# Performance work log

Measured on AMD Instinct MI355X. Metric: run time of the kernel, lower is better.

Reference implementation:

```python
import jax, jax.numpy as jnp
import numpy as np

HEAD_DIM = 1024
SCALE = HEAD_DIM ** -0.25  # qk_scale defaults to exponent -0.25


def setup_inputs() -> dict:
    key = jax.random.key(0)
    ks = jax.random.split(key, 6)
    B_s, B_q, C = 4096, 4096, 1024
    return {
        "query": jax.random.normal(ks[0], (B_q, C), dtype=jnp.float32),
        "s": jax.random.normal(ks[1], (B_s, C), dtype=jnp.float32),
        "TG_prompt": jax.random.normal(ks[2], (B_s, C), dtype=jnp.float32),
        "W_qkv": jax.random.normal(ks[3], (3 * HEAD_DIM, C), dtype=jnp.float32) * (C ** -0.5),
        "W_proj_s": jax.random.normal(ks[4], (HEAD_DIM, HEAD_DIM), dtype=jnp.float32) * (HEAD_DIM ** -0.5),
        "W_proj_q": jax.random.normal(ks[5], (HEAD_DIM, HEAD_DIM), dtype=jnp.float32) * (HEAD_DIM ** -0.5),
    }


def reference(query, s, TG_prompt, W_qkv, W_proj_s, W_proj_q):
    B_s = s.shape[0]
    t = s + TG_prompt                       # [B_s, C]
    c = jnp.concatenate([t, query], axis=0)  # [B, C], B = B_s + B_q
    x = c @ W_qkv.T                          # [B, 3*head_dim]
    q, k, v = jnp.split(x, 3, axis=-1)       # each [B, head_dim]
    # separate sqrt-scale on q and k, then full [B, B] scores
    attn = jax.nn.softmax((q * SCALE) @ (k.T * SCALE), axis=-1)
    attn_cq = attn[:B_s, B_s:]               # [B_s, B_q]
    attn_qc = attn[B_s:, :B_s]               # [B_q, B_s]
    # matmul against raw query / s (NOT v), then per-branch projection
    x_s = (attn_cq @ query) @ W_proj_s.T     # [B_s, head_dim]
    x_q = (attn_qc @ s) @ W_proj_q.T         # [B_q, head_dim]
    return (x_s, x_q)
```

## Files before the change

kernel.cpp:

```cpp
#include <hip/hip_runtime.h>


typedef unsigned short u16;
typedef __bf16 bf16x8 __attribute__((ext_vector_type(8)));
typedef float f32x4 __attribute__((ext_vector_type(4)));
typedef unsigned short u16x8 __attribute__((ext_vector_type(8)));

#define DEVI static __device__ __forceinline__

DEVI u16 f2b(float f) {
  unsigned int u = __float_as_uint(f);
  u += 0x7fffu + ((u >> 16) & 1u);
  return (u16)(u >> 16);
}

DEVI float exp2_hw(float x) {
  float r;
  asm("v_exp_f32 %0, %1" : "=v"(r) : "v"(x));
  return r;
}

__global__ void prep_all(const float* __restrict__ query, const float* __restrict__ s,
                         const float* __restrict__ tg, const float* __restrict__ w0,
                         const float* __restrict__ w1, const float* __restrict__ w2,
                         u16* __restrict__ cB, u16* __restrict__ sBf,
                         u16* __restrict__ o0, u16* __restrict__ o1,
                         u16* __restrict__ o2, float* __restrict__ rowsum) {
  int b = blockIdx.x;
  if (b >= 6144) {
    rowsum[(b - 6144) * 1024 + (int)threadIdx.x * 4 + 0] = 0.f;
    rowsum[(b - 6144) * 1024 + (int)threadIdx.x * 4 + 1] = 0.f;
    rowsum[(b - 6144) * 1024 + (int)threadIdx.x * 4 + 2] = 0.f;
    rowsum[(b - 6144) * 1024 + (int)threadIdx.x * 4 + 3] = 0.f;
    return;
  }
  if (b < 4096) {
    int base = (b * 256 + threadIdx.x) << 3;
    int row = base >> 10;
    u16x8 o;
    if (row < 4096) {
      float4 a0 = *(const float4*)(s + base);
      float4 a1 = *(const float4*)(s + base + 4);
      float4 b0 = *(const float4*)(tg + base);
      float4 b1 = *(const float4*)(tg + base + 4);
      u16x8 os;
      os[0] = f2b(a0.x); os[1] = f2b(a0.y); os[2] = f2b(a0.z); os[3] = f2b(a0.w);
      os[4] = f2b(a1.x); os[5] = f2b(a1.y); os[6] = f2b(a1.z); os[7] = f2b(a1.w);
      *(u16x8*)(sBf + base) = os;
      o[0] = f2b(a0.x + b0.x); o[1] = f2b(a0.y + b0.y);
      o[2] = f2b(a0.z + b0.z); o[3] = f2b(a0.w + b0.w);
      o[4] = f2b(a1.x + b1.x); o[5] = f2b(a1.y + b1.y);
      o[6] = f2b(a1.z + b1.z); o[7] = f2b(a1.w + b1.w);
    } else {
      int qb = base - 4096 * 1024;
      float4 a0 = *(const float4*)(query + qb);
      float4 a1 = *(const float4*)(query + qb + 4);
      o[0] = f2b(a0.x); o[1] = f2b(a0.y); o[2] = f2b(a0.z); o[3] = f2b(a0.w);
      o[4] = f2b(a1.x); o[5] = f2b(a1.y); o[6] = f2b(a1.z); o[7] = f2b(a1.w);
    }
    *(u16x8*)(cB + base) = o;
  } else {
    const float* in; u16* out; int lb;
    if (b < 5120)      { in = w0; out = o0; lb = b - 4096; }
    else if (b < 5632) { in = w1; out = o1; lb = b - 5120; }
    else               { in = w2; out = o2; lb = b - 5632; }
    int base = (lb * 256 + threadIdx.x) << 3;
    float4 a0 = *(const float4*)(in + base);
    float4 a1 = *(const float4*)(in + base + 4);
    u16x8 o;
    o[0] = f2b(a0.x); o[1] = f2b(a0.y); o[2] = f2b(a0.z); o[3] = f2b(a0.w);
    o[4] = f2b(a1.x); o[5] = f2b(a1.y); o[6] = f2b(a1.z); o[7] = f2b(a1.w);
    *(u16x8*)(out + base) = o;
  }
}

__global__ __launch_bounds__(256)
void gemm_qkv(const u16* __restrict__ cB, const u16* __restrict__ WqkB,
              u16* __restrict__ qks,
              const u16* __restrict__ WpsB, const u16* __restrict__ WpqB,
              const u16* __restrict__ qBf, const u16* __restrict__ sBf,
              u16* __restrict__ VsT, u16* __restrict__ VqT,
              float sq, float sk) {
  __shared__ __align__(16) u16 sA[128 * 64];
  __shared__ __align__(16) u16 sB[128 * 64];
  const int b = blockIdx.x;
  const u16* Ap; const u16* Bp; u16* op;
  int bx, by, ldc;
  bool proj;
  if (b < 1024) {
    proj = true;  bx = b & 15; by = b >> 4;
    Ap = cB; Bp = WqkB; op = qks; ldc = 2048;
  } else {
    proj = false;
    int b2 = b - 1024;
    int z = b2 >> 8, rem = b2 & 255;
    bx = rem & 31; by = rem >> 5;
    Ap = z ? WpqB : WpsB; Bp = z ? sBf : qBf; op = z ? VqT : VsT; ldc = 4096;
  }
  const int tid = threadIdx.x;
  const int lane = tid & 63;
  const int wave = tid >> 6;
  const int wr = (wave >> 1) * 64;
  const int wc = (wave & 1) * 64;
  const int ar = lane & 15;

  const u16* Ab = Ap + (size_t)(by * 128) * 1024;
  const u16* Bb = Bp + (size_t)(bx * 128) * 1024;

  f32x4 zero = {0.0f, 0.0f, 0.0f, 0.0f};
  f32x4 acc[4][4];
#pragma unroll
  for (int i = 0; i < 4; ++i)
#pragma unroll
    for (int j = 0; j < 4; ++j) acc[i][j] = zero;

  const int sr = tid >> 3;
  const int scL = (tid & 7) << 3;
  const int scG = ((tid & 7) ^ (sr & 7)) << 3;

  const int l7 = lane & 7, l16 = lane >> 4;
  const int p0b = (l16 ^ l7) << 4;
  const int offA0 = (wr + ar) * 128 + p0b;
  const int offB0 = (wc + ar) * 128 + p0b;
  const char* sAc = (const char*)sA;
  const char* sBc = (const char*)sB;

  for (int k0 = 0; k0 < 1024; k0 += 64) {
#pragma unroll
    for (int it = 0; it < 4; ++it) {
      int r = it * 32 + sr;
      __builtin_amdgcn_global_load_lds(
          (__attribute__((address_space(1))) void*)(Ab + (size_t)r * 1024 + k0 + scG),
          (__attribute__((address_space(3))) void*)(sA + r * 64 + scL), 16, 0, 0);
    }
#pragma unroll
    for (int it = 0; it < 4; ++it) {
      int r = it * 32 + sr;
      __builtin_amdgcn_global_load_lds(
          (__attribute__((address_space(1))) void*)(Bb + (size_t)r * 1024 + k0 + scG),
          (__attribute__((address_space(3))) void*)(sB + r * 64 + scL), 16, 0, 0);
    }
    __syncthreads();
#pragma unroll
    for (int half = 0; half < 2; ++half) {
      const int px = half ? 64 : 0;
      bf16x8 af[4], bfr[4];
#pragma unroll
      for (int t = 0; t < 4; ++t)
        af[t] = *(const bf16x8*)(sAc + ((offA0 ^ px) + t * 2048));
#pragma unroll
      for (int t = 0; t < 4; ++t)
        bfr[t] = *(const bf16x8*)(sBc + ((offB0 ^ px) + t * 2048));
#pragma unroll
      for (int tm = 0; tm < 4; ++tm)
#pragma unroll
        for (int tn = 0; tn < 4; ++tn)
          acc[tm][tn] = __builtin_amdgcn_mfma_f32_16x16x32_bf16(
              af[tm], bfr[tn], acc[tm][tn], 0, 0, 0);
    }
    __syncthreads();
  }

  const int qr = (lane >> 4) * 4;
  const int qc = lane & 15;
#pragma unroll
  for (int tm = 0; tm < 4; ++tm)
#pragma unroll
    for (int r = 0; r < 4; ++r) {
      int row = by * 128 + wr + tm * 16 + qr + r;
#pragma unroll
      for (int tn = 0; tn < 4; ++tn) {
        int col = bx * 128 + wc + tn * 16 + qc;
        float sc = proj ? ((col < 1024) ? sq : sk) : 1.0f;
        op[(size_t)row * ldc + col] = f2b(acc[tm][tn][r] * sc);
      }
    }
}


template <int EPI>
__global__ __launch_bounds__(256)
void gemm_bt(const u16* __restrict__ A, const u16* __restrict__ A1,
             const u16* __restrict__ B, const u16* __restrict__ B1,
             int lda, int ldb, int K, int ldc,
             float* __restrict__ outf, float* __restrict__ outf1,
             const float* __restrict__ rs, const float* __restrict__ rs1,
             u16* __restrict__ Pcq, u16* __restrict__ Pqc,
             float* __restrict__ rowsum) {
  __shared__ __align__(16) u16 sA[128 * 64];
  __shared__ __align__(16) u16 sB[128 * 64];
  const int tid = threadIdx.x;
  const int lane = tid & 63;
  const int wave = tid >> 6;
  const int wr = (wave >> 1) * 64;
  const int wc = (wave & 1) * 64;
  const int ar = lane & 15;
  const int by = blockIdx.y, bx = blockIdx.x;
  const int z = blockIdx.z;

  const u16* Ab = (z ? A1 : A) + (size_t)(by * 128) * lda;
  const u16* Bb = (z ? B1 : B) + (size_t)(bx * 128) * ldb;

  f32x4 zero = {0.0f, 0.0f, 0.0f, 0.0f};
  f32x4 acc[4][4];
#pragma unroll
  for (int i = 0; i < 4; ++i)
#pragma unroll
    for (int j = 0; j < 4; ++j) acc[i][j] = zero;

  const int sr = tid >> 3;
  const int scL = (tid & 7) << 3;
  const int scG = ((tid & 7) ^ (sr & 7)) << 3;

  const int l7 = lane & 7, l16 = lane >> 4;
  const int p0b = (l16 ^ l7) << 4;
  const int offA0 = (wr + ar) * 128 + p0b;
  const int offB0 = (wc + ar) * 128 + p0b;
  const char* sAc = (const char*)sA;
  const char* sBc = (const char*)sB;

  for (int k0 = 0; k0 < K; k0 += 64) {
#pragma unroll
    for (int it = 0; it < 4; ++it) {
      int r = it * 32 + sr;
      __builtin_amdgcn_global_load_lds(
          (__attribute__((address_space(1))) void*)(Ab + (size_t)r * lda + k0 + scG),
          (__attribute__((address_space(3))) void*)(sA + r * 64 + scL), 16, 0, 0);
    }
#pragma unroll
    for (int it = 0; it < 4; ++it) {
      int r = it * 32 + sr;
      __builtin_amdgcn_global_load_lds(
          (__attribute__((address_space(1))) void*)(Bb + (size_t)r * ldb + k0 + scG),
          (__attribute__((address_space(3))) void*)(sB + r * 64 + scL), 16, 0, 0);
    }
    __syncthreads();
#pragma unroll
    for (int half = 0; half < 2; ++half) {
      const int px = half ? 64 : 0;
      bf16x8 af[4], bfr[4];
#pragma unroll
      for (int t = 0; t < 4; ++t)
        af[t] = *(const bf16x8*)(sAc + ((offA0 ^ px) + t * 2048));
#pragma unroll
      for (int t = 0; t < 4; ++t)
        bfr[t] = *(const bf16x8*)(sBc + ((offB0 ^ px) + t * 2048));
#pragma unroll
      for (int tm = 0; tm < 4; ++tm)
#pragma unroll
        for (int tn = 0; tn < 4; ++tn)
          acc[tm][tn] = __builtin_amdgcn_mfma_f32_16x16x32_bf16(
              af[tm], bfr[tn], acc[tm][tn], 0, 0, 0);
    }
    __syncthreads();
  }

  const int qr = (lane >> 4) * 4;
  const int qc = lane & 15;

  if constexpr (EPI == 1) {
    const bool top = (by < 32);
    const bool left = (bx < 32);
    u16* pdst = nullptr;
    if (top && !left) pdst = Pcq;
    if (!top && left) pdst = Pqc;
    const int growb = by * 128 + wr;
    const int rbase = growb - (top ? 0 : 4096);
    const int cbase = bx * 128 + wc - (left ? 0 : 4096);
#pragma unroll
    for (int tm = 0; tm < 4; ++tm) {
      float e[4][4];
      float rsum[4] = {0.f, 0.f, 0.f, 0.f};
#pragma unroll
      for (int tn = 0; tn < 4; ++tn)
#pragma unroll
        for (int r = 0; r < 4; ++r) {
          e[tn][r] = exp2_hw(acc[tm][tn][r]);
          rsum[r] += e[tn][r];
        }
#pragma unroll
      for (int r = 0; r < 4; ++r) {
        float v = rsum[r];
        v += __shfl_xor(v, 1);
        v += __shfl_xor(v, 2);
        v += __shfl_xor(v, 4);
        v += __shfl_xor(v, 8);
        if ((lane & 15) == 0)
          atomicAdd(&rowsum[growb + tm * 16 + qr + r], v);
      }
      if (pdst) {
#pragma unroll
        for (int tn = 0; tn < 4; ++tn)
#pragma unroll
          for (int r = 0; r < 4; ++r) {
            int row = rbase + tm * 16 + qr + r;
            pdst[(size_t)row * 4096 + cbase + tn * 16 + qc] = f2b(e[tn][r]);
          }
      }
    }
  } else {
    float* of = z ? outf1 : outf;
    const float* rsz = z ? rs1 : rs;
#pragma unroll
    for (int tm = 0; tm < 4; ++tm)
#pragma unroll
      for (int r = 0; r < 4; ++r) {
        int row = by * 128 + wr + tm * 16 + qr + r;
        float inv = 1.0f / rsz[row];
#pragma unroll
        for (int tn = 0; tn < 4; ++tn) {
          int col = bx * 128 + wc + tn * 16 + qc;
          of[(size_t)row * ldc + col] = acc[tm][tn][r] * inv;
        }
      }
  }
}


extern "C" void kernel_launch(void* const* d_in, const int* in_sizes, int n_in,
                              void* d_out, int out_size, void* d_ws, size_t ws_size,
                              hipStream_t stream) {
  (void)in_sizes; (void)n_in; (void)out_size; (void)ws_size;
  const float* query = (const float*)d_in[0];
  const float* s     = (const float*)d_in[1];
  const float* tg    = (const float*)d_in[2];
  const float* Wqkv  = (const float*)d_in[3];
  const float* Wps   = (const float*)d_in[4];
  const float* Wpq   = (const float*)d_in[5];
  float* out = (float*)d_out;

  char* ws = (char*)d_ws;
  u16* cB     = (u16*)ws; ws += (size_t)8192 * 1024 * 2;
  u16* sBf    = (u16*)ws; ws += (size_t)4096 * 1024 * 2;
  u16* qks    = (u16*)ws; ws += (size_t)8192 * 2048 * 2;
  u16* WqkB   = (u16*)ws; ws += (size_t)2048 * 1024 * 2;
  u16* WpsB   = (u16*)ws; ws += (size_t)1024 * 1024 * 2;
  u16* WpqB   = (u16*)ws; ws += (size_t)1024 * 1024 * 2;
  u16* VsT    = (u16*)ws; ws += (size_t)1024 * 4096 * 2;
  u16* VqT    = (u16*)ws; ws += (size_t)1024 * 4096 * 2;
  u16* Pcq    = (u16*)ws; ws += (size_t)4096 * 4096 * 2;
  u16* Pqc    = (u16*)ws; ws += (size_t)4096 * 4096 * 2;
  float* rowsum = (float*)ws;

  const u16* qBf = cB + (size_t)4096 * 1024;

  const float SCALE = 0.17677669529663687f;
  const float LOG2E = 1.4426950408889634f;

  prep_all<<<6152, 256, 0, stream>>>(query, s, tg, Wqkv, Wps, Wpq,
                                     cB, sBf, WqkB, WpsB, WpqB, rowsum);
  gemm_qkv<<<1536, 256, 0, stream>>>(cB, WqkB, qks, WpsB, WpqB, qBf, sBf,
                                     VsT, VqT, SCALE * LOG2E, SCALE);
  gemm_bt<1><<<dim3(64, 64), 256, 0, stream>>>(
      qks, nullptr, qks + 1024, nullptr, 2048, 2048, 1024, 0,
      nullptr, nullptr, nullptr, nullptr, Pcq, Pqc, rowsum);
  gemm_bt<4><<<dim3(8, 32, 2), 256, 0, stream>>>(
      Pcq, Pqc, VsT, VqT, 4096, 4096, 4096, 1024,
      out, out + (size_t)4096 * 1024, rowsum, rowsum + 4096,
      nullptr, nullptr, nullptr);
}
```

Baseline: 468.1 us.

## Enlarge GEMM block tiles to 256x128 with 8-wave 512-thread blocks

Factors the shared-memory MFMA K-loop into a helper and doubles the M dimension of every GEMM tile to 256 rows. Blocks grow to 512 threads (8 waves), so each B tile in LDS feeds twice as many rows and global traffic per output drops. Grids, row indexing and the top/bottom split in the softmax epilogue are rescaled to match. The cost is a larger LDS footprint and fewer resident blocks per CU, and the block count halves, which could underfill the GPU on the smaller launches.

```diff
diff --git a/kernel.cpp b/kernel.cpp
--- a/kernel.cpp
+++ b/kernel.cpp
@@ -28,10 +28,8 @@
                          u16* __restrict__ o2, float* __restrict__ rowsum) {
   int b = blockIdx.x;
   if (b >= 6144) {
-    rowsum[(b - 6144) * 1024 + (int)threadIdx.x * 4 + 0] = 0.f;
-    rowsum[(b - 6144) * 1024 + (int)threadIdx.x * 4 + 1] = 0.f;
-    rowsum[(b - 6144) * 1024 + (int)threadIdx.x * 4 + 2] = 0.f;
-    rowsum[(b - 6144) * 1024 + (int)threadIdx.x * 4 + 3] = 0.f;
+    int i = (b - 6144) * 1024 + (int)threadIdx.x * 4;
+    rowsum[i] = 0.f; rowsum[i + 1] = 0.f; rowsum[i + 2] = 0.f; rowsum[i + 3] = 0.f;
     return;
   }
   if (b < 4096) {
@@ -74,26 +72,80 @@
   }
 }
 
-__global__ __launch_bounds__(256)
+struct KLoopOut { f32x4 acc[4][4]; };
+
+DEVI void kloop(const u16* Ab, const u16* Bb, int lda, int ldb, int K,
+                u16* sA, u16* sB, int tid, int wr, int wc, f32x4 (&acc)[4][4]) {
+  const int lane = tid & 63;
+  const int ar = lane & 15;
+  const int sr = tid >> 3;
+  const int scL = (tid & 7) << 3;
+  const int scG = ((tid & 7) ^ (sr & 7)) << 3;
+
+  const int l7 = lane & 7, l16 = lane >> 4;
+  const int p0b = (l16 ^ l7) << 4;
+  const int offA0 = (wr + ar) * 128 + p0b;
+  const int offB0 = (wc + ar) * 128 + p0b;
+  const char* sAc = (const char*)sA;
+  const char* sBc = (const char*)sB;
+
+  for (int k0 = 0; k0 < K; k0 += 64) {
+#pragma unroll
+    for (int it = 0; it < 4; ++it) {
+      int r = it * 64 + sr;
+      __builtin_amdgcn_global_load_lds(
+          (__attribute__((address_space(1))) void*)(Ab + (size_t)r * lda + k0 + scG),
+          (__attribute__((address_space(3))) void*)(sA + r * 64 + scL), 16, 0, 0);
+    }
+#pragma unroll
+    for (int it = 0; it < 2; ++it) {
+      int r = it * 64 + sr;
+      __builtin_amdgcn_global_load_lds(
+          (__attribute__((address_space(1))) void*)(Bb + (size_t)r * ldb + k0 + scG),
+          (__attribute__((address_space(3))) void*)(sB + r * 64 + scL), 16, 0, 0);
+    }
+    __syncthreads();
+#pragma unroll
+    for (int half = 0; half < 2; ++half) {
+      const int px = half ? 64 : 0;
+      bf16x8 af[4], bfr[4];
+#pragma unroll
+      for (int t = 0; t < 4; ++t)
+        af[t] = *(const bf16x8*)(sAc + ((offA0 ^ px) + t * 2048));
+#pragma unroll
+      for (int t = 0; t < 4; ++t)
+        bfr[t] = *(const bf16x8*)(sBc + ((offB0 ^ px) + t * 2048));
+#pragma unroll
+      for (int tm = 0; tm < 4; ++tm)
+#pragma unroll
+        for (int tn = 0; tn < 4; ++tn)
+          acc[tm][tn] = __builtin_amdgcn_mfma_f32_16x16x32_bf16(
+              af[tm], bfr[tn], acc[tm][tn], 0, 0, 0);
+    }
+    __syncthreads();
+  }
+}
+
+__global__ __launch_bounds__(512)
 void gemm_qkv(const u16* __restrict__ cB, const u16* __restrict__ WqkB,
               u16* __restrict__ qks,
               const u16* __restrict__ WpsB, const u16* __restrict__ WpqB,
               const u16* __restrict__ qBf, const u16* __restrict__ sBf,
               u16* __restrict__ VsT, u16* __restrict__ VqT,
               float sq, float sk) {
-  __shared__ __align__(16) u16 sA[128 * 64];
+  __shared__ __align__(16) u16 sA[256 * 64];
   __shared__ __align__(16) u16 sB[128 * 64];
   const int b = blockIdx.x;
   const u16* Ap; const u16* Bp; u16* op;
   int bx, by, ldc;
   bool proj;
-  if (b < 1024) {
+  if (b < 512) {
     proj = true;  bx = b & 15; by = b >> 4;
     Ap = cB; Bp = WqkB; op = qks; ldc = 2048;
   } else {
     proj = false;
-    int b2 = b - 1024;
-    int z = b2 >> 8, rem = b2 & 255;
+    int b2 = b - 512;
+    int z = b2 >> 7, rem = b2 & 127;
     bx = rem & 31; by = rem >> 5;
     Ap = z ? WpqB : WpsB; Bp = z ? sBf : qBf; op = z ? VqT : VsT; ldc = 4096;
   }
@@ -102,64 +154,15 @@
   const int wave = tid >> 6;
   const int wr = (wave >> 1) * 64;
   const int wc = (wave & 1) * 64;
-  const int ar = lane & 15;
-
-  const u16* Ab = Ap + (size_t)(by * 128) * 1024;
-  const u16* Bb = Bp + (size_t)(bx * 128) * 1024;
-
-  f32x4 zero = {0.0f, 0.0f, 0.0f, 0.0f};
+
   f32x4 acc[4][4];
 #pragma unroll
   for (int i = 0; i < 4; ++i)
 #pragma unroll
-    for (int j = 0; j < 4; ++j) acc[i][j] = zero;
-
-  const int sr = tid >> 3;
-  const int scL = (tid & 7) << 3;
-  const int scG = ((tid & 7) ^ (sr & 7)) << 3;
-
-  const int l7 = lane & 7, l16 = lane >> 4;
-  const int p0b = (l16 ^ l7) << 4;
-  const int offA0 = (wr + ar) * 128 + p0b;
-  const int offB0 = (wc + ar) * 128 + p0b;
-  const char* sAc = (const char*)sA;
-  const char* sBc = (const char*)sB;
-
-  for (int k0 = 0; k0 < 1024; k0 += 64) {
-#pragma unroll
-    for (int it = 0; it < 4; ++it) {
-      int r = it * 32 + sr;
-      __builtin_amdgcn_global_load_lds(
-          (__attribute__((address_space(1))) void*)(Ab + (size_t)r * 1024 + k0 + scG),
-          (__attribute__((address_space(3))) void*)(sA + r * 64 + scL), 16, 0, 0);
-    }
-#pragma unroll
-    for (int it = 0; it < 4; ++it) {
-      int r = it * 32 + sr;
-      __builtin_amdgcn_global_load_lds(
-          (__attribute__((address_space(1))) void*)(Bb + (size_t)r * 1024 + k0 + scG),
-          (__attribute__((address_space(3))) void*)(sB + r * 64 + scL), 16, 0, 0);
-    }
-    __syncthreads();
-#pragma unroll
-    for (int half = 0; half < 2; ++half) {
-      const int px = half ? 64 : 0;
-      bf16x8 af[4], bfr[4];
-#pragma unroll
-      for (int t = 0; t < 4; ++t)
-        af[t] = *(const bf16x8*)(sAc + ((offA0 ^ px) + t * 2048));
-#pragma unroll
-      for (int t = 0; t < 4; ++t)
-        bfr[t] = *(const bf16x8*)(sBc + ((offB0 ^ px) + t * 2048));
-#pragma unroll
-      for (int tm = 0; tm < 4; ++tm)
-#pragma unroll
-        for (int tn = 0; tn < 4; ++tn)
-          acc[tm][tn] = __builtin_amdgcn_mfma_f32_16x16x32_bf16(
-              af[tm], bfr[tn], acc[tm][tn], 0, 0, 0);
-    }
-    __syncthreads();
-  }
+    for (int j = 0; j < 4; ++j) acc[i][j] = f32x4{0.f, 0.f, 0.f, 0.f};
+
+  kloop(Ap + (size_t)(by * 256) * 1024, Bp + (size_t)(bx * 128) * 1024,
+        1024, 1024, 1024, sA, sB, tid, wr, wc, acc);
 
   const int qr = (lane >> 4) * 4;
   const int qc = lane & 15;
@@ -167,7 +170,7 @@
   for (int tm = 0; tm < 4; ++tm)
 #pragma unroll
     for (int r = 0; r < 4; ++r) {
-      int row = by * 128 + wr + tm * 16 + qr + r;
+      int row = by * 256 + wr + tm * 16 + qr + r;
 #pragma unroll
       for (int tn = 0; tn < 4; ++tn) {
         int col = bx * 128 + wc + tn * 16 + qc;
@@ -177,9 +180,8 @@
     }
 }
 
-
 template <int EPI>
-__global__ __launch_bounds__(256)
+__global__ __launch_bounds__(512)
 void gemm_bt(const u16* __restrict__ A, const u16* __restrict__ A1,
              const u16* __restrict__ B, const u16* __restrict__ B1,
              int lda, int ldb, int K, int ldc,
@@ -187,84 +189,36 @@
              const float* __restrict__ rs, const float* __restrict__ rs1,
              u16* __restrict__ Pcq, u16* __restrict__ Pqc,
              float* __restrict__ rowsum) {
-  __shared__ __align__(16) u16 sA[128 * 64];
+  __shared__ __align__(16) u16 sA[256 * 64];
   __shared__ __align__(16) u16 sB[128 * 64];
   const int tid = threadIdx.x;
   const int lane = tid & 63;
   const int wave = tid >> 6;
   const int wr = (wave >> 1) * 64;
   const int wc = (wave & 1) * 64;
-  const int ar = lane & 15;
   const int by = blockIdx.y, bx = blockIdx.x;
   const int z = blockIdx.z;
 
-  const u16* Ab = (z ? A1 : A) + (size_t)(by * 128) * lda;
-  const u16* Bb = (z ? B1 : B) + (size_t)(bx * 128) * ldb;
-
-  f32x4 zero = {0.0f, 0.0f, 0.0f, 0.0f};
   f32x4 acc[4][4];
 #pragma unroll
   for (int i = 0; i < 4; ++i)
 #pragma unroll
-    for (int j = 0; j < 4; ++j) acc[i][j] = zero;
-
-  const int sr = tid >> 3;
-  const int scL = (tid & 7) << 3;
-  const int scG = ((tid & 7) ^ (sr & 7)) << 3;
-
-  const int l7 = lane & 7, l16 = lane >> 4;
-  const int p0b = (l16 ^ l7) << 4;
-  const int offA0 = (wr + ar) * 128 + p0b;
-  const int offB0 = (wc + ar) * 128 + p0b;
-  const char* sAc = (const char*)sA;
-  const char* sBc = (const char*)sB;
-
-  for (int k0 = 0; k0 < K; k0 += 64) {
-#pragma unroll
-    for (int it = 0; it < 4; ++it) {
-      int r = it * 32 + sr;
-      __builtin_amdgcn_global_load_lds(
-          (__attribute__((address_space(1))) void*)(Ab + (size_t)r * lda + k0 + scG),
-          (__attribute__((address_space(3))) void*)(sA + r * 64 + scL), 16, 0, 0);
-    }
-#pragma unroll
-    for (int it = 0; it < 4; ++it) {
-      int r = it * 32 + sr;
-      __builtin_amdgcn_global_load_lds(
-          (__attribute__((address_space(1))) void*)(Bb + (size_t)r * ldb + k0 + scG),
-          (__attribute__((address_space(3))) void*)(sB + r * 64 + scL), 16, 0, 0);
-    }
-    __syncthreads();
-#pragma unroll
-    for (int half = 0; half < 2; ++half) {
-      const int px = half ? 64 : 0;
-      bf16x8 af[4], bfr[4];
-#pragma unroll
-      for (int t = 0; t < 4; ++t)
-        af[t] = *(const bf16x8*)(sAc + ((offA0 ^ px) + t * 2048));
-#pragma unroll
-      for (int t = 0; t < 4; ++t)
-        bfr[t] = *(const bf16x8*)(sBc + ((offB0 ^ px) + t * 2048));
-#pragma unroll
-      for (int tm = 0; tm < 4; ++tm)
-#pragma unroll
-        for (int tn = 0; tn < 4; ++tn)
-          acc[tm][tn] = __builtin_amdgcn_mfma_f32_16x16x32_bf16(
-              af[tm], bfr[tn], acc[tm][tn], 0, 0, 0);
-    }
-    __syncthreads();
-  }
+    for (int j = 0; j < 4; ++j) acc[i][j] = f32x4{0.f, 0.f, 0.f, 0.f};
+
+  kloop((z ? A1 : A) + (size_t)(by * 256) * lda,
+        (z ? B1 : B) + (size_t)(bx * 128) * ldb,
+        lda, ldb, K, sA, sB, tid, wr, wc, acc);
 
   const int qr = (lane >> 4) * 4;
   const int qc = lane & 15;
 
   if constexpr (EPI == 1) {
-    const bool top = (by < 32);
+    const bool top = (by < 16);
     const bool left = (bx < 32);
     u16* pdst = nullptr;
     if (top && !left) pdst = Pcq;
     if (!top && left) pdst = Pqc;
-    const int growb = by * 128 + wr;
+    const int growb = by * 256 + wr;
     const int rbase = growb - (top ? 0 : 4096);
     const int cbase = bx * 128 + wc - (left ? 0 : 4096);
 #pragma unroll
@@ -305,7 +259,7 @@
     for (int tm = 0; tm < 4; ++tm)
 #pragma unroll
       for (int r = 0; r < 4; ++r) {
-        int row = by * 128 + wr + tm * 16 + qr + r;
+        int row = by * 256 + wr + tm * 16 + qr + r;
         float inv = 1.0f / rsz[row];
 #pragma unroll
         for (int tn = 0; tn < 4; ++tn) {
@@ -349,12 +303,12 @@
 
   prep_all<<<6152, 256, 0, stream>>>(query, s, tg, Wqkv, Wps, Wpq,
                                      cB, sBf, WqkB, WpsB, WpqB, rowsum);
-  gemm_qkv<<<1536, 256, 0, stream>>>(cB, WqkB, qks, WpsB, WpqB, qBf, sBf,
-                                     VsT, VqT, SCALE * LOG2E, SCALE);
-  gemm_bt<1><<<dim3(64, 64), 256, 0, stream>>>(
+  gemm_qkv<<<768, 512, 0, stream>>>(cB, WqkB, qks, WpsB, WpqB, qBf, sBf,
+                                    VsT, VqT, SCALE * LOG2E, SCALE);
+  gemm_bt<1><<<dim3(64, 32), 512, 0, stream>>>(
       qks, nullptr, qks + 1024, nullptr, 2048, 2048, 1024, 0,
       nullptr, nullptr, nullptr, nullptr, Pcq, Pqc, rowsum);
-  gemm_bt<4><<<dim3(8, 32, 2), 256, 0, stream>>>(
+  gemm_bt<4><<<dim3(8, 16, 2), 512, 0, stream>>>(
       Pcq, Pqc, VsT, VqT, 4096, 4096, 4096, 1024,
       out, out + (size_t)4096 * 1024, rowsum, rowsum + 4096,
       nullptr, nullptr, nullptr);
```

Result: faster. 444.6 us (-5.0%).
